# Optimization experiments

Hardware: AMD Instinct MI355X
Metric: run time of the kernel (lower is better)

The kernel has to match this reference:

```python
import jax, jax.numpy as jnp
import numpy as np

N_NODES = 100000
N_EDGES = 1600000
D_IN = 128
D_OUT = 128


def setup_inputs() -> dict:
    key = jax.random.key(0)
    k1, k2, k3, k4, k5 = jax.random.split(key, 5)
    x = jax.random.normal(k1, (N_NODES, D_IN), dtype=jnp.float32)
    # nn.Linear(in, out, bias=False) weight has shape [out, in]
    W = jax.random.normal(k2, (D_OUT, D_IN), dtype=jnp.float32) * (1.0 / np.sqrt(D_IN))
    edge_vals = jax.random.uniform(k3, (N_EDGES,), dtype=jnp.float32)
    edge_src = jax.random.randint(k4, (N_EDGES,), 0, N_NODES, dtype=jnp.int32)
    edge_dst = jax.random.randint(k5, (N_EDGES,), 0, N_NODES, dtype=jnp.int32)
    return {"x": x, "W": W, "edge_vals": edge_vals,
            "edge_src": edge_src, "edge_dst": edge_dst}


def reference(x, W, edge_vals, edge_src, edge_dst):
    # 1) linear projection (no bias): h = x @ W^T  -> [N, D_OUT]
    h = jnp.dot(x, W.T)
    # 2) sparse adjacency SpMM: out[i] = sum_{e: dst=i} vals[e] * h[src[e]]
    msgs = edge_vals[:, None] * h[edge_src]          # [E, D_OUT]
    agg = jax.ops.segment_sum(msgs, edge_dst, num_segments=N_NODES)
    # 3) exact GELU (torch.nn.GELU default)
    return jax.nn.gelu(agg, approximate=False)
```

## Files before the change

kernel.cpp:

```cpp
#include <hip/hip_runtime.h>
#include <math.h>

#define NN 100000
#define NE 1600000
#define D 128

#define NB 782
#define CAPB 2560
#define CURSTRIDE 16
#define SC_BLOCKS 512
#define SC_CHUNK 3125
#define SC_IT 13
#define CAP 768

#define BM 64
#define GM_BLOCKS 1563
#define GRID (SC_BLOCKS + GM_BLOCKS)
#define TPAD 264

#define ASG __attribute__((address_space(1)))
#define ASL __attribute__((address_space(3)))

typedef __attribute__((ext_vector_type(8))) short bf16x8;
typedef __attribute__((ext_vector_type(4))) float f32x4;
typedef __attribute__((ext_vector_type(4))) unsigned int u32x4;

__device__ __forceinline__ unsigned int cvt_pk_bf16(float lo, float hi) {
    unsigned int r;
    asm("v_cvt_pk_bf16_f32 %0, %1, %2" : "=v"(r) : "v"(lo), "v"(hi));
    return r;
}

__global__ __launch_bounds__(256) void wconv_kernel(const float* __restrict__ W,
                                                    unsigned short* __restrict__ Wswz,
                                                    int* __restrict__ bucketCursor) {
    int i = blockIdx.x * 256 + threadIdx.x;
    int r = i >> 4, s = i & 15;
    const float4* wp = reinterpret_cast<const float4*>(W + (size_t)r * D + s * 8);
    float4 v0 = wp[0], v1 = wp[1];
    uint2 a, b;
    a.x = cvt_pk_bf16(v0.x, v0.y); a.y = cvt_pk_bf16(v0.z, v0.w);
    b.x = cvt_pk_bf16(v1.x, v1.y); b.y = cvt_pk_bf16(v1.z, v1.w);
    int so = s ^ (r & 15);
    unsigned short* op = Wswz + (size_t)r * D + so * 8;
    *reinterpret_cast<uint2*>(op)     = a;
    *reinterpret_cast<uint2*>(op + 4) = b;
    for (int z = i; z < NB * CURSTRIDE; z += 2048) bucketCursor[z] = 0;
}

__global__ __launch_bounds__(256) void gemm_scatter_kernel(const float* __restrict__ x,
                                                           const unsigned short* __restrict__ Wswz,
                                                           unsigned short* __restrict__ h,
                                                           const int* __restrict__ src,
                                                           const int* __restrict__ dst,
                                                           const float* __restrict__ vals,
                                                           int* __restrict__ bucketCursor,
                                                           uint2* __restrict__ ebuf) {
    __shared__ __align__(16) unsigned char smem[40960];
    const int tid = threadIdx.x;
    const int lane = tid & 63;
    const int w = tid >> 6;
    const int g = blockIdx.x;

    if (g < SC_BLOCKS) {
        uint2* s_rec        = reinterpret_cast<uint2*>(smem);
        int*   l_off        = reinterpret_cast<int*>(smem + 25000);
        int*   l_cur        = reinterpret_cast<int*>(smem + 28128);
        int*   l_cnt        = reinterpret_cast<int*>(smem + 31256);
        int*   wtot         = reinterpret_cast<int*>(smem + 34384);
        unsigned short* s_b = reinterpret_cast<unsigned short*>(smem + 34400);

        const int t = tid;
        const int cb = g * SC_CHUNK;

        for (int i = t; i < NB; i += 256) l_cnt[i] = 0;
        __syncthreads();

        int dreg[SC_IT];
#pragma unroll
        for (int i = 0; i < SC_IT; ++i) {
            int o = t + 256 * i;
            dreg[i] = (o < SC_CHUNK) ? dst[cb + o] : -1;
            if (dreg[i] >= 0) atomicAdd(&l_cnt[dreg[i] >> 7], 1);
        }
        __syncthreads();

        int c[4];
        int s = 0;
#pragma unroll
        for (int i = 0; i < 4; ++i) {
            int b = 4 * t + i;
            c[i] = (b < NB) ? l_cnt[b] : 0;
            s += c[i];
        }
        int incl = s;
#pragma unroll
        for (int off = 1; off < 64; off <<= 1) {
            int v = __shfl_up(incl, off);
            if (lane >= off) incl += v;
        }
        if (lane == 63) wtot[w] = incl;
        __syncthreads();
        int run = incl - s;
        for (int k = 0; k < 4; ++k) if (k < w) run += wtot[k];
#pragma unroll
        for (int i = 0; i < 4; ++i) {
            int b = 4 * t + i;
            if (b < NB) {
                l_cur[b] = run;
                int gbase = b * CAPB +
                    (c[i] ? atomicAdd(&bucketCursor[b * CURSTRIDE], c[i]) : 0);
                l_off[b] = gbase - run;
            }
            run += c[i];
        }
        __syncthreads();

#pragma unroll
        for (int i = 0; i < SC_IT; ++i) {
            int o = t + 256 * i;
            if (dreg[i] >= 0) {
                int dn = dreg[i];
                int b = dn >> 7;
                uint2 rec;
                rec.x = (unsigned int)src[cb + o] | ((unsigned int)(dn & 127) << 17);
                rec.y = __float_as_uint(vals[cb + o]);
                int lofs = atomicAdd(&l_cur[b], 1);
                s_rec[lofs] = rec;
                s_b[lofs] = (unsigned short)b;
            }
        }
        __syncthreads();

#pragma unroll
        for (int i = 0; i < SC_IT; ++i) {
            int j = t + 256 * i;
            if (j < SC_CHUNK) {
                int b = s_b[j];
                ebuf[l_off[b] + j] = s_rec[j];
            }
        }
    } else {
        unsigned char* lBbuf = smem;
        const int rowBase = (g - SC_BLOCKS) * BM;

#pragma unroll
        for (int q = 0; q < 8; ++q) {
            const unsigned char* gp = reinterpret_cast<const unsigned char*>(Wswz)
                                      + (size_t)((w * 8 + q) * 1024 + lane * 16);
            unsigned char* lp = lBbuf + (w * 8 + q) * 1024;
            __builtin_amdgcn_global_load_lds((ASG const unsigned int*)(const void*)gp,
                                             (ASL unsigned int*)(void*)lp, 16, 0, 0);
        }

        const int l16 = lane & 15;
        const int arow = min(rowBase + w * 16 + l16, NN - 1);
        const float* xrow = x + (size_t)arow * D + (lane >> 4) * 8;

        bf16x8 afr[4];
#pragma unroll
        for (int kk = 0; kk < 4; ++kk) {
            float4 v0 = *reinterpret_cast<const float4*>(xrow + kk * 32);
            float4 v1 = *reinterpret_cast<const float4*>(xrow + kk * 32 + 4);
            u32x4 u;
            u[0] = cvt_pk_bf16(v0.x, v0.y);
            u[1] = cvt_pk_bf16(v0.z, v0.w);
            u[2] = cvt_pk_bf16(v1.x, v1.y);
            u[3] = cvt_pk_bf16(v1.z, v1.w);
            afr[kk] = __builtin_bit_cast(bf16x8, u);
        }
        __syncthreads();

        const int kx16 = (lane >> 4) * 16;
        f32x4 acc[8];
#pragma unroll
        for (int j = 0; j < 8; ++j) acc[j] = (f32x4){0.f, 0.f, 0.f, 0.f};

        const int bxor = l16 << 4;
#pragma unroll
        for (int kk = 0; kk < 4; ++kk) {
            int kbyte = kk * 64 + kx16;
#pragma unroll
            for (int j = 0; j < 8; ++j) {
                int row = j * 16 + l16;
                bf16x8 b = *reinterpret_cast<const bf16x8*>(
                    lBbuf + row * 256 + (kbyte ^ bxor));
                acc[j] = __builtin_amdgcn_mfma_f32_16x16x32_bf16(afr[kk], b, acc[j], 0, 0, 0);
            }
        }
        __syncthreads();

        const int lr0 = w * 16 + (lane >> 4) * 4;
#pragma unroll
        for (int j = 0; j < 8; ++j) {
            int col = j * 16 + l16;
            unsigned int d01 = cvt_pk_bf16(acc[j][0], acc[j][1]);
            unsigned int d23 = cvt_pk_bf16(acc[j][2], acc[j][3]);
            unsigned char* p0 = lBbuf + lr0 * TPAD + col * 2;
            *reinterpret_cast<unsigned short*>(p0)            = (unsigned short)d01;
            *reinterpret_cast<unsigned short*>(p0 + TPAD)     = (unsigned short)(d01 >> 16);
            *reinterpret_cast<unsigned short*>(p0 + 2 * TPAD) = (unsigned short)d23;
            *reinterpret_cast<unsigned short*>(p0 + 3 * TPAD) = (unsigned short)(d23 >> 16);
        }
        __syncthreads();

#pragma unroll
        for (int i = 0; i < 8; ++i) {
            int f = tid + 256 * i;
            int r = f >> 5, c = f & 31;
            if (rowBase + r < NN) {
                uint2 v = *reinterpret_cast<const uint2*>(lBbuf + r * TPAD + c * 8);
                *reinterpret_cast<uint2*>(reinterpret_cast<unsigned char*>(h)
                                          + (size_t)(rowBase + r) * 256 + c * 8) = v;
            }
        }
    }
}

__global__ __launch_bounds__(256) void pull_kernel(const unsigned short* __restrict__ h,
                                                   const int* __restrict__ bucketCursor,
                                                   const uint2* __restrict__ ebuf,
                                                   float* __restrict__ out) {
    __shared__ uint2 srec[CAP];
    __shared__ int cnt[32];
    __shared__ int start[33];
    __shared__ int cur[32];
    __shared__ __align__(16) unsigned char hbuf[4 * 4096];

    const int t = threadIdx.x;
    const int lane = t & 63;
    const int w = t >> 6;
    const int bid = blockIdx.x;
    const int b = bid >> 2;
    const int quarter = bid & 3;
    const int nodeBase = b * 128 + quarter * 32;

    unsigned char* hbufW = hbuf + w * 4096;

    float2 acc[8];
#pragma unroll
    for (int i = 0; i < 8; ++i) acc[i] = (float2){0.f, 0.f};

    const int n = min(bucketCursor[b * CURSTRIDE], CAPB);
    const uint2* eb = ebuf + (size_t)b * CAPB;

    if (t < 32) cnt[t] = 0;
    __syncthreads();

    uint2 rcache[10];
#pragma unroll
    for (int it = 0; it < 10; ++it) {
        int j = t + 256 * it;
        uint2 r = (j < n) ? eb[j] : (uint2){0xFFFFFFFFu, 0u};
        rcache[it] = r;
        if (j < n) {
            int dl = (int)((r.x >> 17) & 127);
            if ((dl >> 5) == quarter) atomicAdd(&cnt[dl & 31], 1);
        }
    }
    __syncthreads();

    if (w == 0) {
        int c = (lane < 32) ? cnt[lane] : 0;
        int s = c;
        for (int off = 1; off < 32; off <<= 1) {
            int v = __shfl_up(s, off);
            if (lane >= off) s += v;
        }
        if (lane < 32) { start[lane] = s - c; cur[lane] = s - c; }
        if (lane == 31) start[32] = s;
    }
    __syncthreads();

#pragma unroll
    for (int it = 0; it < 10; ++it) {
        int j = t + 256 * it;
        if (j < n) {
            uint2 rec = rcache[it];
            int dl = (int)((rec.x >> 17) & 127);
            if ((dl >> 5) == quarter) {
                int p = atomicAdd(&cur[dl & 31], 1);
                srec[p] = rec;
            }
        }
    }
    __syncthreads();

    const int wbeg = start[w * 8];
    const int wend = start[w * 8 + 8];
    int issued = 0;
    int consumed = 0;

    auto issue_group = [&]() {
        int gbase = wbeg + issued * 8;
#pragma unroll
        for (int q = 0; q < 2; ++q) {
            int idx = min(gbase + q * 4 + (lane >> 4), wend - 1);
            unsigned int rx = reinterpret_cast<const unsigned int*>(&srec[idx])[0];
            const unsigned char* gp = reinterpret_cast<const unsigned char*>(h)
                                      + (size_t)(rx & 0x1FFFFu) * 256 + (size_t)((lane & 15) * 16);
            unsigned char* lp = hbufW + (issued & 1) * 2048 + q * 1024;
            __builtin_amdgcn_global_load_lds((ASG const unsigned int*)(const void*)gp,
                                             (ASL unsigned int*)(void*)lp, 16, 0, 0);
        }
        issued++;
    };

    if (wend > wbeg) { issue_group(); issue_group(); }

    int gate = wbeg;
    const unsigned char* hp = hbufW + lane * 4;
    const unsigned char* vp = reinterpret_cast<const unsigned char*>(srec) + (size_t)wbeg * 8 + 4;

#pragma unroll
    for (int i = 0; i < 8; ++i) {
        const int s1 = start[w * 8 + i + 1];
        float2 a = acc[i];
        for (int e = start[w * 8 + i]; e < s1; ++e) {
            if (e >= gate) {
                if (consumed) issue_group();
                asm volatile("s_waitcnt vmcnt(2)" ::: "memory");
                __builtin_amdgcn_sched_barrier(0);
                hp = hbufW + (consumed & 1) * 2048 + lane * 4;
                consumed++;
                gate += 8;
            }
            unsigned int hw = *reinterpret_cast<const unsigned int*>(hp);
            float v = *reinterpret_cast<const float*>(vp);
            hp += 256;
            vp += 8;
            a.x = fmaf(v, __uint_as_float(hw << 16), a.x);
            a.y = fmaf(v, __uint_as_float(hw & 0xFFFF0000u), a.y);
        }
        acc[i] = a;
    }
    __syncthreads();

    const float is2 = 0.70710678118654752f;
#pragma unroll
    for (int i = 0; i < 8; ++i) {
        int node = nodeBase + w * 8 + i;
        if (node < NN) {
            float a0 = acc[i].x, a1 = acc[i].y;
            a0 = 0.5f * a0 * (1.f + erff(a0 * is2));
            a1 = 0.5f * a1 * (1.f + erff(a1 * is2));
            float2 o; o.x = a0; o.y = a1;
            *reinterpret_cast<float2*>(out + (size_t)node * D + lane * 2) = o;
        }
    }
}

extern "C" void kernel_launch(void* const* d_in, const int* in_sizes, int n_in,
                              void* d_out, int out_size, void* d_ws, size_t ws_size,
                              hipStream_t stream) {
    const float* x    = (const float*)d_in[0];
    const float* W    = (const float*)d_in[1];
    const float* vals = (const float*)d_in[2];
    const int*   src  = (const int*)d_in[3];
    const int*   dst  = (const int*)d_in[4];
    float* out = (float*)d_out;

    char* ws = (char*)d_ws;
    size_t off = 0;
    unsigned short* h    = (unsigned short*)(ws + off); off += (size_t)NN * D * 2;
    int* bucketCursor    = (int*)(ws + off);            off += (size_t)NB * CURSTRIDE * 4;
    off = (off + 15) & ~(size_t)15;
    unsigned short* Wswz = (unsigned short*)(ws + off); off += (size_t)D * D * 2;
    off = (off + 15) & ~(size_t)15;
    uint2* ebuf          = (uint2*)(ws + off);          off += (size_t)NB * CAPB * 8;

    wconv_kernel<<<8, 256, 0, stream>>>(W, Wswz, bucketCursor);
    gemm_scatter_kernel<<<GRID, 256, 0, stream>>>(
        x, Wswz, h, src, dst, vals, bucketCursor, ebuf);
    pull_kernel<<<NB * 4, 256, 0, stream>>>(h, bucketCursor, ebuf, out);
}
```

Baseline: 125.4 us.

## Split each wavefront into half-waves processing two edges per step with 8-byte LDS reads

```diff
diff --git a/kernel.cpp b/kernel.cpp
--- a/kernel.cpp
+++ b/kernel.cpp
@@ -221,7 +221,7 @@
                                                    const int* __restrict__ bucketCursor,
                                                    const uint2* __restrict__ ebuf,
                                                    float* __restrict__ out) {
-    __shared__ uint2 srec[CAP];
+    __shared__ uint2 srec[CAP + 1];
     __shared__ int cnt[32];
     __shared__ int start[33];
     __shared__ int cur[32];
@@ -236,10 +236,6 @@
     const int nodeBase = b * 128 + quarter * 32;
 
     unsigned char* hbufW = hbuf + w * 4096;
-
-    float2 acc[8];
-#pragma unroll
-    for (int i = 0; i < 8; ++i) acc[i] = (float2){0.f, 0.f};
 
     const int n = min(bucketCursor[b * CURSTRIDE], CAPB);
     const uint2* eb = ebuf + (size_t)b * CAPB;
@@ -288,6 +284,8 @@
 
     const int wbeg = start[w * 8];
     const int wend = start[w * 8 + 8];
+    const int lh  = lane >> 5;
+    const int l31 = lane & 31;
     int issued = 0;
     int consumed = 0;
 
@@ -309,43 +307,72 @@
     if (wend > wbeg) { issue_group(); issue_group(); }
 
     int gate = wbeg;
-    const unsigned char* hp = hbufW + lane * 4;
-    const unsigned char* vp = reinterpret_cast<const unsigned char*>(srec) + (size_t)wbeg * 8 + 4;
+    const unsigned char* slotbase = hbufW;
+    const unsigned int* srec_dw = reinterpret_cast<const unsigned int*>(srec);
+
+    float4 acc4[8];
+#pragma unroll
+    for (int i = 0; i < 8; ++i) acc4[i] = (float4){0.f, 0.f, 0.f, 0.f};
 
 #pragma unroll
     for (int i = 0; i < 8; ++i) {
         const int s1 = start[w * 8 + i + 1];
-        float2 a = acc[i];
-        for (int e = start[w * 8 + i]; e < s1; ++e) {
+        int e = start[w * 8 + i];
+        float4 a = acc4[i];
+        while (e < s1) {
             if (e >= gate) {
                 if (consumed) issue_group();
                 asm volatile("s_waitcnt vmcnt(2)" ::: "memory");
                 __builtin_amdgcn_sched_barrier(0);
-                hp = hbufW + (consumed & 1) * 2048 + lane * 4;
+                slotbase = hbufW + (consumed & 1) * 2048;
                 consumed++;
                 gate += 8;
             }
-            unsigned int hw = *reinterpret_cast<const unsigned int*>(hp);
-            float v = *reinterpret_cast<const float*>(vp);
-            hp += 256;
-            vp += 8;
-            a.x = fmaf(v, __uint_as_float(hw << 16), a.x);
-            a.y = fmaf(v, __uint_as_float(hw & 0xFFFF0000u), a.y);
-        }
-        acc[i] = a;
+            const int lim = min(s1, gate);
+            for (; e + 1 < lim; e += 2) {
+                int le = e - wbeg;
+                uint2 hw2 = *reinterpret_cast<const uint2*>(
+                    slotbase + ((le + lh) & 7) * 256 + l31 * 8);
+                float v = __uint_as_float(srec_dw[(e + lh) * 2 + 1]);
+                a.x = fmaf(v, __uint_as_float(hw2.x << 16),         a.x);
+                a.y = fmaf(v, __uint_as_float(hw2.x & 0xFFFF0000u), a.y);
+                a.z = fmaf(v, __uint_as_float(hw2.y << 16),         a.z);
+                a.w = fmaf(v, __uint_as_float(hw2.y & 0xFFFF0000u), a.w);
+            }
+            if (e < lim) {
+                int le = e - wbeg;
+                uint2 hw2 = *reinterpret_cast<const uint2*>(
+                    slotbase + ((le + lh) & 7) * 256 + l31 * 8);
+                float v = __uint_as_float(srec_dw[(e + lh) * 2 + 1]);
+                if (lh) v = 0.f;
+                a.x = fmaf(v, __uint_as_float(hw2.x << 16),         a.x);
+                a.y = fmaf(v, __uint_as_float(hw2.x & 0xFFFF0000u), a.y);
+                a.z = fmaf(v, __uint_as_float(hw2.y << 16),         a.z);
+                a.w = fmaf(v, __uint_as_float(hw2.y & 0xFFFF0000u), a.w);
+                ++e;
+            }
+        }
+        acc4[i] = a;
     }
     __syncthreads();
 
     const float is2 = 0.70710678118654752f;
 #pragma unroll
     for (int i = 0; i < 8; ++i) {
-        int node = nodeBase + w * 8 + i;
-        if (node < NN) {
-            float a0 = acc[i].x, a1 = acc[i].y;
-            a0 = 0.5f * a0 * (1.f + erff(a0 * is2));
-            a1 = 0.5f * a1 * (1.f + erff(a1 * is2));
-            float2 o; o.x = a0; o.y = a1;
-            *reinterpret_cast<float2*>(out + (size_t)node * D + lane * 2) = o;
+        float4 o;
+        o.x = acc4[i].x + __shfl_xor(acc4[i].x, 32);
+        o.y = acc4[i].y + __shfl_xor(acc4[i].y, 32);
+        o.z = acc4[i].z + __shfl_xor(acc4[i].z, 32);
+        o.w = acc4[i].w + __shfl_xor(acc4[i].w, 32);
+        if (lh == (i & 1)) {
+            int node = nodeBase + w * 8 + i;
+            if (node < NN) {
+                o.x = 0.5f * o.x * (1.f + erff(o.x * is2));
+                o.y = 0.5f * o.y * (1.f + erff(o.y * is2));
+                o.z = 0.5f * o.z * (1.f + erff(o.z * is2));
+                o.w = 0.5f * o.w * (1.f + erff(o.w * is2));
+                *reinterpret_cast<float4*>(out + (size_t)node * D + l31 * 4) = o;
+            }
         }
     }
 }
```

Result: slower. 130.6 us (+4.1%).
